# Performance work log

Hardware: AMD Instinct MI355X
Metric: run time of the kernel (lower is better)

## Reference

```python
import jax, jax.numpy as jnp
import numpy as np

# static sinkhorn parameters (match SamplesLoss init kwargs)
P = 2
BLUR = 0.05
SCALING = 0.5
DIAMETER = 2.0  # points on the unit sphere => diameter <= 2

# geomloss epsilon_schedule: [diameter^p] + exp(arange(p*log(d), p*log(blur), p*log(scaling))) + [blur^p]
EPS_LIST = (
    [DIAMETER ** P]
    + [float(np.exp(e)) for e in np.arange(P * np.log(DIAMETER), P * np.log(BLUR), P * np.log(SCALING))]
    + [BLUR ** P]
)


def cost(m, n):
    # spherical (geodesic) distance / 2 between unit vectors: acos(<m,n>)/2
    t = jnp.clip(jnp.einsum('bnd,bmd->bnm', m, n), -1.0 + 1e-6, 1.0 - 1e-6)
    return jnp.arccos(t) * 0.5  # (B,N,M)


def softmin(eps, C, wlog):
    # -eps * logsumexp(wlog[B,1,M] - C/eps, axis=2) -> (B,N)
    return -eps * jax.nn.logsumexp(wlog[:, None, :] - C / eps, axis=2)


def log_weights(a):
    return jnp.where(a > 0, jnp.log(jnp.maximum(a, 1e-30)), -1e5)


def setup_inputs() -> dict:
    key = jax.random.key(0)
    kx, ky = jax.random.split(key)
    B, N, M, D = 8, 2048, 2048, 3
    x = jax.random.normal(kx, (B, N, D), dtype=jnp.float32)
    y = jax.random.normal(ky, (B, M, D), dtype=jnp.float32)
    # project onto the unit sphere (spherical cost assumes unit vectors)
    x = x / jnp.linalg.norm(x, axis=-1, keepdims=True)
    y = y / jnp.linalg.norm(y, axis=-1, keepdims=True)
    alpha = jnp.ones((B, N), dtype=jnp.float32) / N
    beta = jnp.ones((B, M), dtype=jnp.float32) / M
    return {"alpha": alpha, "x": x, "beta": beta, "y": y}


def reference(alpha, x, beta, y):
    sg = jax.lax.stop_gradient
    # second argument of each cost is detached, as in the torch code
    C_xx = cost(x, sg(x))
    C_yy = cost(y, sg(y))
    C_xy = cost(x, sg(y))
    C_yx = cost(y, sg(x))
    al = log_weights(alpha)
    bl = log_weights(beta)

    # ---- sinkhorn loop (torch.no_grad section) ----
    Cxx_, Cyy_, Cxy_, Cyx_, al_, bl_ = map(sg, (C_xx, C_yy, C_xy, C_yx, al, bl))
    eps = EPS_LIST[0]
    a_x = softmin(eps, Cxx_, al_)   # OT(a,a) potential on x
    b_y = softmin(eps, Cyy_, bl_)   # OT(b,b) potential on y
    a_y = softmin(eps, Cyx_, al_)   # OT(a,b) potential on y
    b_x = softmin(eps, Cxy_, bl_)   # OT(a,b) potential on x
    for eps in EPS_LIST:  # annealed, symmetrized sinkhorn updates
        at_x = softmin(eps, Cxx_, al_ + a_x / eps)
        bt_y = softmin(eps, Cyy_, bl_ + b_y / eps)
        at_y = softmin(eps, Cyx_, al_ + b_x / eps)
        bt_x = softmin(eps, Cxy_, bl_ + a_y / eps)
        a_x, b_y = 0.5 * (a_x + at_x), 0.5 * (b_y + bt_y)
        a_y, b_x = 0.5 * (a_y + at_y), 0.5 * (b_x + bt_x)

    # ---- last extrapolation, differentiable (eps = blur^p) ----
    eps = EPS_LIST[-1]
    a_x = softmin(eps, C_xx, sg(al + a_x / eps))
    b_y = softmin(eps, C_yy, sg(bl + b_y / eps))
    a_y = softmin(eps, C_yx, sg(al + b_x / eps))
    b_x = softmin(eps, C_xy, sg(bl + a_y / eps))

    # balanced (reach=None), debiased sinkhorn cost -> (B,)
    return jnp.sum(alpha * (b_x - a_x), axis=-1) + jnp.sum(beta * (a_y - b_y), axis=-1)
```

## Files before the change

### kernel.cpp

```cpp
#include <hip/hip_runtime.h>
#include <math.h>

#define BB 8
#define NN 2048
#define L2E 1.4426950408889634f
#define LN2 0.6931471805599453f
#define PI_F 3.14159265358979f
#define CLIP 0.999999f
#define THSC 20860.0f
#define THSCI (1.0f / 20860.0f)

constexpr int TB   = 128;
constexpr int T16  = NN / TB;
constexpr int NXX  = T16 * (T16 + 1) / 2;
constexpr int NT   = 2 * NXX + T16 * T16;
constexpr int SARR = BB * NN;

__device__ __forceinline__ void decode_tile(int bx, int& kind, int& I, int& J) {
    if (bx < NXX) kind = 0;
    else if (bx < 2 * NXX) { kind = 1; bx -= NXX; }
    else { kind = 2; bx -= 2 * NXX; }
    if (kind < 2) {
        int idx = bx; I = 0;
        for (;;) { int len = T16 - I; if (idx < len) { J = I + idx; break; } idx -= len; I++; }
    } else { I = bx >> 4; J = bx & 15; }
}

__device__ __forceinline__ float acos_raw(float d) {
    const float u = fabsf(d);
    float pl = fmaf(u, -0.0187293f, 0.0742610f);
    pl = fmaf(u, pl, -0.2121144f); pl = fmaf(u, pl, 1.5707288f);
    const float rt = __builtin_amdgcn_sqrtf(1.f - u) * pl;
    return (d >= 0.f) ? rt : (PI_F - rt);
}

__device__ __forceinline__ size_t th_off(int g, int wv, int lane) {
    return (size_t)(((g * 4 + wv) * 64 + lane) * 8);
}

__global__ __launch_bounds__(256)
void pack_kernel(const float* __restrict__ alpha, const float* __restrict__ beta,
                 float* __restrict__ gxw, float* __restrict__ gyw,
                 float* __restrict__ Wall, float* __restrict__ Gall)
{
    const int tid = threadIdx.x;
    const int gid = blockIdx.x * 256 + tid;
    const int o = gid >> 14, i = gid & (SARR - 1);
    const float* w = (o == 0 || o == 3) ? alpha : beta;
    const float v = w[i];
    const float g = ((v > 0.f) ? logf(fmaxf(v, 1e-30f)) : -1e5f) * L2E;
    if (o == 0) gxw[i] = g;
    if (o == 1) gyw[i] = g;
    __shared__ float red[256];
    red[tid] = g;
    __syncthreads();
    const int base = tid & 128, loc = tid & 127;
    for (int st = 64; st; st >>= 1) {
        if (loc < st) red[base + loc] = fmaxf(red[base + loc], red[base + loc + st]);
        __syncthreads();
    }
    const float G = red[base];
    Wall[gid] = __builtin_amdgcn_exp2f(g - G);
    if (loc == 0) Gall[gid >> 7] = G;
}

__global__ __launch_bounds__(256)
void maxes_kernel(const float* __restrict__ x, const float* __restrict__ y,
                  float* __restrict__ Rxx, float* __restrict__ Ryy,
                  float* __restrict__ Rxy, float* __restrict__ Cxy,
                  unsigned short* __restrict__ Theta,
                  const float* __restrict__ Wall, const float* __restrict__ Gall,
                  float2* pAX, float2* pBY, float2* pAY, float2* pBX,
                  float negK, int writeTheta)
{
    __shared__ float4 p1s[TB], p2s[TB];
    __shared__ float colred[4][TB];
    __shared__ float colpart[4][TB];
    int kind, I, J; decode_tile(blockIdx.x, kind, I, J);
    const int b = blockIdx.y, t = threadIdx.x;
    const float* P1 = (kind == 1) ? y : x;
    const float* P2 = (kind == 0) ? x : y;
    const int o1 = (kind == 0) ? 0 : (kind == 1) ? 1 : 3;
    const int o2 = (kind == 0) ? 0 : (kind == 1) ? 1 : 2;
    float2* rowOut = (kind == 0) ? pAX : (kind == 1) ? pBY : pBX;
    float2* colOut = (kind == 0) ? pAX : (kind == 1) ? pBY : pAY;
    const bool diag = (kind < 2) && (I == J);
    const float* W1 = Wall + (size_t)o1 * SARR;
    const float* W2 = Wall + (size_t)o2 * SARR;

    if (t < TB) {
        size_t gi = (size_t)b * NN + (size_t)I * TB + t;
        p1s[t] = make_float4(P1[gi * 3], P1[gi * 3 + 1], P1[gi * 3 + 2], W1[gi]);
    } else {
        int u = t - TB; size_t gi = (size_t)b * NN + (size_t)J * TB + u;
        p2s[u] = make_float4(P2[gi * 3], P2[gi * 3 + 1], P2[gi * 3 + 2], W2[gi]);
    }
    const float G1 = Gall[o1 * 128 + b * T16 + I];
    const float G2 = Gall[o2 * 128 + b * T16 + J];
    __syncthreads();
    const int lane = t & 63, wv = t >> 6, colg = lane & 7, rowg = lane >> 3;
    const int r0 = wv * 32 + rowg * 4;
    unsigned short* Tb = Theta + ((size_t)(b * NT + blockIdx.x) << 14);

    float4 pr[4];
#pragma unroll
    for (int rr = 0; rr < 4; rr++) pr[rr] = p1s[r0 + rr];
    float rmx[4] = {-2.f, -2.f, -2.f, -2.f};
    float cmx[16];
#pragma unroll
    for (int j = 0; j < 16; j++) cmx[j] = -2.f;
    float racc[4] = {0.f, 0.f, 0.f, 0.f};
    float cacc[16];
#pragma unroll
    for (int j = 0; j < 16; j++) cacc[j] = 0.f;

#pragma unroll
    for (int g = 0; g < 8; g++) {
        uint4 outv;
#pragma unroll
        for (int e = 0; e < 2; e++) {
            const int j = g * 2 + e;
            const float4 q = p2s[colg + 8 * j];
            unsigned int lo = 0, hi = 0;
#pragma unroll
            for (int rr = 0; rr < 4; rr++) {
                const float d = fmaf(pr[rr].x, q.x, fmaf(pr[rr].y, q.y, pr[rr].z * q.z));
                rmx[rr] = fmaxf(rmx[rr], d);
                cmx[j] = fmaxf(cmx[j], d);
                if (writeTheta) {
                    const float dc = fminf(fmaxf(d, -CLIP), CLIP);
                    const float th = acos_raw(dc);
                    const unsigned int qv = __float2uint_rn(th * THSC);
                    if (rr == 0) lo = qv;
                    else if (rr == 1) lo |= qv << 16;
                    else if (rr == 2) hi = qv;
                    else hi |= qv << 16;
                    const float em = __builtin_amdgcn_exp2f(th * negK);
                    racc[rr] = fmaf(q.w, em, racc[rr]);
                    cacc[j]  = fmaf(pr[rr].w, em, cacc[j]);
                }
            }
            if (e == 0) { outv.x = lo; outv.y = hi; }
            else        { outv.z = lo; outv.w = hi; }
        }
        if (writeTheta)
            *(uint4*)(Tb + th_off(g, wv, lane)) = outv;
    }

#pragma unroll
    for (int rr = 0; rr < 4; rr++) {
        float v = rmx[rr];
        v = fmaxf(v, __shfl_xor(v, 1)); v = fmaxf(v, __shfl_xor(v, 2));
        v = fmaxf(v, __shfl_xor(v, 4));
        rmx[rr] = v;
    }
    if (colg == 0) {
        float* R = (kind == 0) ? Rxx : (kind == 1) ? Ryy : Rxy;
        const size_t base = ((size_t)b * T16 + J) * NN + (size_t)I * TB + r0;
#pragma unroll
        for (int rr = 0; rr < 4; rr++)
            R[base + rr] = acos_raw(fminf(fmaxf(rmx[rr], -CLIP), CLIP));
    }
#pragma unroll
    for (int j = 0; j < 16; j++) {
        float v = cmx[j];
        v = fmaxf(v, __shfl_xor(v, 8)); v = fmaxf(v, __shfl_xor(v, 16));
        v = fmaxf(v, __shfl_xor(v, 32));
        cmx[j] = v;
    }
    if (rowg == 0) {
#pragma unroll
        for (int j = 0; j < 16; j++) colred[wv][colg + 8 * j] = cmx[j];
    }

    if (writeTheta) {
#pragma unroll
        for (int j = 0; j < 16; j++) {
            float v = cacc[j];
            v += __shfl_xor(v, 8); v += __shfl_xor(v, 16); v += __shfl_xor(v, 32);
            cacc[j] = v;
        }
        if (rowg == 0) {
#pragma unroll
            for (int j = 0; j < 16; j++) colpart[wv][colg + 8 * j] = cacc[j];
        }
#pragma unroll
        for (int rr = 0; rr < 4; rr++) {
            float v = racc[rr];
            v += __shfl_xor(v, 1); v += __shfl_xor(v, 2); v += __shfl_xor(v, 4);
            racc[rr] = v;
        }
        if (colg == 0) {
            const size_t gr = (size_t)J * SARR + (size_t)b * NN + (size_t)I * TB + r0;
#pragma unroll
            for (int rr = 0; rr < 4; rr++)
                rowOut[gr + rr] = make_float2(G2, racc[rr]);
        }
    }

    __syncthreads();
    if (t < TB) {
        const float v = fmaxf(fmaxf(colred[0][t], colred[1][t]),
                              fmaxf(colred[2][t], colred[3][t]));
        const float th = acos_raw(fminf(fmaxf(v, -CLIP), CLIP));
        if (kind == 2) {
            Cxy[((size_t)b * T16 + I) * NN + (size_t)J * TB + t] = th;
        } else if (I != J) {
            float* R = (kind == 0) ? Rxx : Ryy;
            R[((size_t)b * T16 + I) * NN + (size_t)J * TB + t] = th;
        }
        if (writeTheta && !diag) {
            const float pv = colpart[0][t] + colpart[1][t] + colpart[2][t] + colpart[3][t];
            const size_t gc = (size_t)I * SARR + (size_t)b * NN + (size_t)J * TB + t;
            colOut[gc] = make_float2(G1, pv);
        }
    }
}

struct TileArgsT {
    const unsigned short* Theta;
    const float* Wall; const float* Gall;
    const float* Rxx; const float* Ryy; const float* Rxy; const float* Cxy;
    float2* pAX; float2* pBY; float2* pAY; float2* pBX;
};

__global__ __launch_bounds__(256)
void tile_theta_kernel(TileArgsT A, float ieh, float Kq)
{
    __shared__ float2 s1[TB];
    __shared__ float2 wq2[TB];
    __shared__ float  scF[TB];
    __shared__ float  wps[TB];
    __shared__ float colpart[4][TB];
    int kind, I, J; decode_tile(blockIdx.x, kind, I, J);
    const int b = blockIdx.y, t = threadIdx.x;
    const int o1 = (kind == 0) ? 0 : (kind == 1) ? 1 : 3;
    const int o2 = (kind == 0) ? 0 : (kind == 1) ? 1 : 2;
    float2* rowOut = (kind == 0) ? A.pAX : (kind == 1) ? A.pBY : A.pBX;
    float2* colOut = (kind == 0) ? A.pAX : (kind == 1) ? A.pBY : A.pAY;
    const bool diag = (kind < 2) && (I == J);
    const float* W1 = A.Wall + (size_t)o1 * SARR;
    const float* W2 = A.Wall + (size_t)o2 * SARR;
    const float* Rrow = (kind == 0) ? A.Rxx : (kind == 1) ? A.Ryy : A.Rxy;
    const float* Csrc = (kind == 0) ? A.Rxx : (kind == 1) ? A.Ryy : A.Cxy;

    float myW = 0.f, mySc = 0.f;
    if (t < TB) {
        size_t gi = (size_t)b * NN + (size_t)I * TB + t;
        myW = W1[gi];
        s1[t] = make_float2(Rrow[((size_t)b * T16 + J) * NN + (size_t)I * TB + t] * ieh, myW);
    } else {
        int u = t - TB; size_t gi = (size_t)b * NN + (size_t)J * TB + u;
        myW = W2[gi];
        mySc = Csrc[((size_t)b * T16 + I) * NN + (size_t)J * TB + u] * ieh;
        scF[u] = mySc;
    }
    const float G1 = A.Gall[o1 * 128 + b * T16 + I];
    const float G2 = A.Gall[o2 * 128 + b * T16 + J];
    __syncthreads();
    const float Z2 = 0.5f * s1[0].x;
    if (t < TB) {
        wps[t] = myW * __builtin_amdgcn_exp2f(Z2 - 0.5f * s1[t].x);
    } else {
        int u = t - TB;
        wq2[u] = make_float2(0.5f * mySc,
                             myW * __builtin_amdgcn_exp2f(Z2 - 0.5f * mySc));
    }
    __syncthreads();

    const int lane = t & 63, wv = t >> 6, colg = lane & 7, rowg = lane >> 3;
    const int r0 = wv * 32 + rowg * 4;
    const unsigned short* Tb = A.Theta + ((size_t)(b * NT + blockIdx.x) << 14);

    float srrF[4], srr2[4], wpr[4];
#pragma unroll
    for (int rr = 0; rr < 4; rr++) {
        srrF[rr] = s1[r0 + rr].x;
        srr2[rr] = 0.5f * srrF[rr];
        wpr[rr]  = wps[r0 + rr];
    }
    float racc[4] = {0.f, 0.f, 0.f, 0.f};
    float cacc[16];
#pragma unroll
    for (int j = 0; j < 16; j++) cacc[j] = 0.f;

#pragma unroll
    for (int g = 0; g < 8; g++) {
        const uint4 tq = *(const uint4*)(Tb + th_off(g, wv, lane));
#pragma unroll
        for (int e = 0; e < 2; e++) {
            const int j = g * 2 + e;
            const unsigned int lo = e ? tq.z : tq.x;
            const unsigned int hi = e ? tq.w : tq.y;
            const float2 q2 = wq2[colg + 8 * j];
            const float thv[4] = {
                (float)(lo & 0xffffu), (float)(lo >> 16),
                (float)(hi & 0xffffu), (float)(hi >> 16)
            };
            float bs[4];
#pragma unroll
            for (int rr = 0; rr < 4; rr++) bs[rr] = srr2[rr] + q2.x;
#pragma unroll
            for (int rr = 0; rr < 4; rr++) {
                const float em = __builtin_amdgcn_exp2f(fmaf(thv[rr], -Kq, bs[rr]));
                racc[rr] = fmaf(q2.y, em, racc[rr]);
                cacc[j]  = fmaf(wpr[rr], em, cacc[j]);
            }
        }
    }

#pragma unroll
    for (int j = 0; j < 16; j++) {
        float v = cacc[j];
        v += __shfl_xor(v, 8); v += __shfl_xor(v, 16); v += __shfl_xor(v, 32);
        cacc[j] = v;
    }
    if (rowg == 0) {
#pragma unroll
        for (int j = 0; j < 16; j++) {
            const int c = colg + 8 * j;
            colpart[wv][c] = cacc[j] * __builtin_amdgcn_exp2f(wq2[c].x - Z2);
        }
    }
#pragma unroll
    for (int rr = 0; rr < 4; rr++) {
        float v = racc[rr];
        v += __shfl_xor(v, 1); v += __shfl_xor(v, 2); v += __shfl_xor(v, 4);
        racc[rr] = v;
    }
    if (colg == 0) {
        const size_t gr = (size_t)J * SARR + (size_t)b * NN + (size_t)I * TB + r0;
#pragma unroll
        for (int rr = 0; rr < 4; rr++)
            rowOut[gr + rr] = make_float2(G2 - srrF[rr],
                racc[rr] * __builtin_amdgcn_exp2f(srr2[rr] - Z2));
    }
    __syncthreads();
    if (!diag && t < TB) {
        const float v = colpart[0][t] + colpart[1][t] + colpart[2][t] + colpart[3][t];
        const size_t gc = (size_t)I * SARR + (size_t)b * NN + (size_t)J * TB + t;
        colOut[gc] = make_float2(G1 - scF[t], v);
    }
}

struct TileArgs {
    const float* x; const float* y;
    const float* Wall; const float* Gall;
    const float* Rxx; const float* Ryy; const float* Rxy; const float* Cxy;
    float2* pAX; float2* pBY; float2* pAY; float2* pBX;
};

__global__ __launch_bounds__(256)
void tile_kernel(TileArgs A, float ieh, float pi_ieh)
{
    __shared__ float4 p1s[TB], p2s[TB];
    __shared__ float srs[TB], scs[TB];
    __shared__ float colpart[4][TB];
    int kind, I, J; decode_tile(blockIdx.x, kind, I, J);
    const int b = blockIdx.y, t = threadIdx.x;
    const float* P1 = (kind == 1) ? A.y : A.x;
    const float* P2 = (kind == 0) ? A.x : A.y;
    const int o1 = (kind == 0) ? 0 : (kind == 1) ? 1 : 3;
    const int o2 = (kind == 0) ? 0 : (kind == 1) ? 1 : 2;
    float2* rowOut = (kind == 0) ? A.pAX : (kind == 1) ? A.pBY : A.pBX;
    float2* colOut = (kind == 0) ? A.pAX : (kind == 1) ? A.pBY : A.pAY;
    const bool diag = (kind < 2) && (I == J);
    const float* W1 = A.Wall + (size_t)o1 * SARR;
    const float* W2 = A.Wall + (size_t)o2 * SARR;
    const float* Rrow = (kind == 0) ? A.Rxx : (kind == 1) ? A.Ryy : A.Rxy;
    const float* Csrc = (kind == 0) ? A.Rxx : (kind == 1) ? A.Ryy : A.Cxy;

    const float K0 = 1.5707288f * ieh, K1 = -0.2121144f * ieh;
    const float K2 = 0.0742610f * ieh, K3 = -0.0187293f * ieh;

    if (t < TB) {
        size_t gi = (size_t)b * NN + (size_t)I * TB + t;
        p1s[t] = make_float4(P1[gi * 3], P1[gi * 3 + 1], P1[gi * 3 + 2], W1[gi]);
        srs[t] = Rrow[((size_t)b * T16 + J) * NN + (size_t)I * TB + t] * ieh;
    } else {
        int u = t - TB; size_t gi = (size_t)b * NN + (size_t)J * TB + u;
        p2s[u] = make_float4(P2[gi * 3], P2[gi * 3 + 1], P2[gi * 3 + 2], W2[gi]);
        scs[u] = Csrc[((size_t)b * T16 + I) * NN + (size_t)J * TB + u] * ieh;
    }
    const float G1 = A.Gall[o1 * 128 + b * T16 + I];
    const float G2 = A.Gall[o2 * 128 + b * T16 + J];
    __syncthreads();

    const int lane = t & 63, wv = t >> 6, colg = lane & 7, rowg = lane >> 3;
    const int r0 = wv * 32 + rowg * 4;
    float4 pr[4]; float srr[4];
#pragma unroll
    for (int rr = 0; rr < 4; rr++) { pr[rr] = p1s[r0 + rr]; srr[rr] = srs[r0 + rr]; }
    float racc[4] = {0.f, 0.f, 0.f, 0.f};
    float cacc[16];
#pragma unroll
    for (int j = 0; j < 16; j++) cacc[j] = 0.f;

#pragma unroll
    for (int j = 0; j < 16; j++) {
        const float4 q = p2s[colg + 8 * j];
        const float sc = scs[colg + 8 * j];
#pragma unroll
        for (int rr = 0; rr < 4; rr++) {
            const float4 p = pr[rr];
            float d = fmaf(p.x, q.x, fmaf(p.y, q.y, p.z * q.z));
            d = fminf(fmaxf(d, -CLIP), CLIP);
            const float u = fabsf(d);
            float pl = fmaf(u, K3, K2); pl = fmaf(u, pl, K1); pl = fmaf(u, pl, K0);
            const float rt = __builtin_amdgcn_sqrtf(1.f - u) * pl;
            const float ach = (d >= 0.f) ? rt : (pi_ieh - rt);
            racc[rr] = fmaf(q.w, __builtin_amdgcn_exp2f(srr[rr] - ach), racc[rr]);
            cacc[j]  = fmaf(p.w, __builtin_amdgcn_exp2f(sc - ach), cacc[j]);
        }
    }

#pragma unroll
    for (int j = 0; j < 16; j++) {
        float v = cacc[j];
        v += __shfl_xor(v, 8); v += __shfl_xor(v, 16); v += __shfl_xor(v, 32);
        cacc[j] = v;
    }
    if (rowg == 0) {
#pragma unroll
        for (int j = 0; j < 16; j++) colpart[wv][colg + 8 * j] = cacc[j];
    }
#pragma unroll
    for (int rr = 0; rr < 4; rr++) {
        float v = racc[rr];
        v += __shfl_xor(v, 1); v += __shfl_xor(v, 2); v += __shfl_xor(v, 4);
        racc[rr] = v;
    }
    if (colg == 0) {
        const size_t gr = (size_t)J * SARR + (size_t)b * NN + (size_t)I * TB + r0;
#pragma unroll
        for (int rr = 0; rr < 4; rr++)
            rowOut[gr + rr] = make_float2(G2 - srr[rr], racc[rr]);
    }
    __syncthreads();
    if (!diag && t < TB) {
        const float v = colpart[0][t] + colpart[1][t] + colpart[2][t] + colpart[3][t];
        const size_t gc = (size_t)I * SARR + (size_t)b * NN + (size_t)J * TB + t;
        colOut[gc] = make_float2(G1 - scs[t], v);
    }
}

__global__ __launch_bounds__(256)
void combine_kernel(const float2* __restrict__ pAX, const float2* __restrict__ pBY,
                    const float2* __restrict__ pAY, const float2* __restrict__ pBX,
                    float* __restrict__ ax, float* __restrict__ by,
                    float* __restrict__ ay, float* __restrict__ bx,
                    const float* __restrict__ gxw, const float* __restrict__ gyw,
                    float* __restrict__ Wall, float* __restrict__ Gall,
                    float eps_ln2, float nieL2E, int do_avg)
{
    const int tid = threadIdx.x;
    const int gid = blockIdx.x * 256 + tid;
    const int o = gid >> 14, i = gid & (SARR - 1);
    const float2* P = (o == 0) ? pAX : (o == 1) ? pBY : (o == 2) ? pAY : pBX;
    float* pot = (o == 0) ? ax : (o == 1) ? by : (o == 2) ? ay : bx;
    float2 pr[T16];
#pragma unroll
    for (int u = 0; u < T16; u++) pr[u] = P[(size_t)u * SARR + i];
    float M = -3.0e38f;
#pragma unroll
    for (int u = 0; u < T16; u++) M = fmaxf(M, (pr[u].y > 0.f) ? pr[u].x : -3.0e38f);
    float S = 0.f;
#pragma unroll
    for (int u = 0; u < T16; u++)
        S += pr[u].y * __builtin_amdgcn_exp2f(fminf(pr[u].x - M, 0.f));
    S = fmaxf(S, 1e-38f);
    float r = -eps_ln2 * (M + __builtin_amdgcn_logf(S));
    if (do_avg) r = 0.5f * (r + pot[i]);
    pot[i] = r;
    const float g = ((o == 0 || o == 3) ? gxw[i] : gyw[i]) + r * nieL2E;
    __shared__ float red[256];
    red[tid] = g;
    __syncthreads();
    const int base = tid & 128, loc = tid & 127;
    for (int st = 64; st; st >>= 1) {
        if (loc < st) red[base + loc] = fmaxf(red[base + loc], red[base + loc + st]);
        __syncthreads();
    }
    const float G = red[base];
    Wall[gid] = __builtin_amdgcn_exp2f(g - G);
    if (loc == 0) Gall[gid >> 7] = G;
}

__global__ __launch_bounds__(256)
void reduce_kernel(const float* __restrict__ alpha, const float* __restrict__ beta,
                   const float* __restrict__ a_x, const float* __restrict__ b_x,
                   const float* __restrict__ a_y, const float* __restrict__ b_y,
                   float* __restrict__ out)
{
    const int b = blockIdx.x, tid = threadIdx.x;
    float acc = 0.f;
    for (int n = tid; n < NN; n += 256) {
        const size_t i = (size_t)b * NN + n;
        acc += alpha[i] * (b_x[i] - a_x[i]);
        acc += beta[i] * (a_y[i] - b_y[i]);
    }
    __shared__ float red[256];
    red[tid] = acc;
    __syncthreads();
    for (int st = 128; st > 0; st >>= 1) {
        if (tid < st) red[tid] += red[tid + st];
        __syncthreads();
    }
    if (tid == 0) out[b] = red[0];
}

extern "C" void kernel_launch(void* const* d_in, const int* in_sizes, int n_in,
                              void* d_out, int out_size, void* d_ws, size_t ws_size,
                              hipStream_t stream)
{
    const float* alpha = (const float*)d_in[0];
    const float* x     = (const float*)d_in[1];
    const float* beta  = (const float*)d_in[2];
    const float* y     = (const float*)d_in[3];
    float* out = (float*)d_out;
    float* ws  = (float*)d_ws;

    const size_t S = SARR;
    float* gxw  = ws;
    float* gyw  = ws + S;
    float* ax   = ws + 2 * S;
    float* by   = ws + 3 * S;
    float* ay   = ws + 4 * S;
    float* bx   = ws + 5 * S;
    float* Wall = ws + 6 * S;
    float* Gall = ws + 10 * S;
    float* Rxx  = ws + 10 * S + 512;
    float* Ryy  = Rxx + 16 * S;
    float* Rxy  = Ryy + 16 * S;
    float* Cxy  = Rxy + 16 * S;
    float* pb   = Cxy + 16 * S;
    const size_t PSZ = (size_t)SARR * T16;
    float2* pAX = (float2*)pb;
    float2* pBY = pAX + PSZ;
    float2* pAY = pBY + PSZ;
    float2* pBX = pAY + PSZ;

    float* thetaF = pb + (size_t)8 * PSZ;
    unsigned short* Theta = (unsigned short*)thetaF;
    const size_t used_bytes  = (size_t)((char*)thetaF - (char*)ws);
    const size_t theta_bytes = (size_t)BB * NT * 16384 * sizeof(unsigned short);
    const int useTheta = (ws_size >= used_bytes + theta_bytes) ? 1 : 0;

    const float EPS[8] = {4.0f, 4.0f, 1.0f, 0.25f, 0.0625f, 0.015625f, 0.00390625f, 0.0025f};

    pack_kernel<<<(4 * SARR) / 256, 256, 0, stream>>>(alpha, beta, gxw, gyw, Wall, Gall);
    const float negK = -0.5f * (1.f / EPS[0]) * L2E;
    maxes_kernel<<<dim3(NT, BB), 256, 0, stream>>>(x, y, Rxx, Ryy, Rxy, Cxy, Theta,
                                                   Wall, Gall, pAX, pBY, pAY, pBX,
                                                   negK, useTheta);

    TileArgsT TT;
    TT.Theta = Theta; TT.Wall = Wall; TT.Gall = Gall;
    TT.Rxx = Rxx; TT.Ryy = Ryy; TT.Rxy = Rxy; TT.Cxy = Cxy;
    TT.pAX = pAX; TT.pBY = pBY; TT.pAY = pAY; TT.pBX = pBX;

    TileArgs TA;
    TA.x = x; TA.y = y; TA.Wall = Wall; TA.Gall = Gall;
    TA.Rxx = Rxx; TA.Ryy = Ryy; TA.Rxy = Rxy; TA.Cxy = Cxy;
    TA.pAX = pAX; TA.pBY = pBY; TA.pAY = pAY; TA.pBX = pBX;

    auto step = [&](float e, float next_e, int avg, int run_tile) {
        const float ieh = 0.5f * (1.f / e) * L2E;
        if (run_tile) {
            if (useTheta)
                tile_theta_kernel<<<dim3(NT, BB), 256, 0, stream>>>(TT, ieh, ieh * THSCI);
            else
                tile_kernel<<<dim3(NT, BB), 256, 0, stream>>>(TA, ieh, PI_F * ieh);
        }
        combine_kernel<<<(4 * SARR) / 256, 256, 0, stream>>>(
            pAX, pBY, pAY, pBX, ax, by, ay, bx, gxw, gyw, Wall, Gall,
            e * LN2, (1.f / next_e) * L2E, avg);
    };

    step(EPS[0], EPS[0], 0, useTheta ? 0 : 1);
    for (int k = 0; k < 8; k++) step(EPS[k], (k < 7) ? EPS[k + 1] : EPS[7], 1, 1);
    step(EPS[7], EPS[7], 0, 1);

    reduce_kernel<<<BB, 256, 0, stream>>>(alpha, beta, ax, bx, ay, by, out);
}
```

Baseline: 451.8 us.

## Use wave-shuffle max reductions and drop the rank-one exponent factorization in theta tiles

```diff
diff --git a/kernel.cpp b/kernel.cpp
--- a/kernel.cpp
+++ b/kernel.cpp
@@ -51,17 +51,18 @@
     const float g = ((v > 0.f) ? logf(fmaxf(v, 1e-30f)) : -1e5f) * L2E;
     if (o == 0) gxw[i] = g;
     if (o == 1) gyw[i] = g;
-    __shared__ float red[256];
-    red[tid] = g;
-    __syncthreads();
-    const int base = tid & 128, loc = tid & 127;
-    for (int st = 64; st; st >>= 1) {
-        if (loc < st) red[base + loc] = fmaxf(red[base + loc], red[base + loc + st]);
-        __syncthreads();
-    }
-    const float G = red[base];
+    float m = g;
+    m = fmaxf(m, __shfl_xor(m, 1));  m = fmaxf(m, __shfl_xor(m, 2));
+    m = fmaxf(m, __shfl_xor(m, 4));  m = fmaxf(m, __shfl_xor(m, 8));
+    m = fmaxf(m, __shfl_xor(m, 16)); m = fmaxf(m, __shfl_xor(m, 32));
+    __shared__ float wmax[4];
+    const int wv = tid >> 6;
+    if ((tid & 63) == 0) wmax[wv] = m;
+    __syncthreads();
+    const int grp = tid >> 7;
+    const float G = fmaxf(wmax[grp * 2], wmax[grp * 2 + 1]);
     Wall[gid] = __builtin_amdgcn_exp2f(g - G);
-    if (loc == 0) Gall[gid >> 7] = G;
+    if ((tid & 127) == 0) Gall[gid >> 7] = G;
 }
 
 __global__ __launch_bounds__(256)
@@ -227,10 +228,7 @@
 __global__ __launch_bounds__(256)
 void tile_theta_kernel(TileArgsT A, float ieh, float Kq)
 {
-    __shared__ float2 s1[TB];
-    __shared__ float2 wq2[TB];
-    __shared__ float  scF[TB];
-    __shared__ float  wps[TB];
+    __shared__ float2 s1[TB], s2[TB];
     __shared__ float colpart[4][TB];
     int kind, I, J; decode_tile(blockIdx.x, kind, I, J);
     const int b = blockIdx.y, t = threadIdx.x;
@@ -244,41 +242,24 @@
     const float* Rrow = (kind == 0) ? A.Rxx : (kind == 1) ? A.Ryy : A.Rxy;
     const float* Csrc = (kind == 0) ? A.Rxx : (kind == 1) ? A.Ryy : A.Cxy;
 
-    float myW = 0.f, mySc = 0.f;
     if (t < TB) {
         size_t gi = (size_t)b * NN + (size_t)I * TB + t;
-        myW = W1[gi];
-        s1[t] = make_float2(Rrow[((size_t)b * T16 + J) * NN + (size_t)I * TB + t] * ieh, myW);
+        s1[t] = make_float2(Rrow[((size_t)b * T16 + J) * NN + (size_t)I * TB + t] * ieh, W1[gi]);
     } else {
         int u = t - TB; size_t gi = (size_t)b * NN + (size_t)J * TB + u;
-        myW = W2[gi];
-        mySc = Csrc[((size_t)b * T16 + I) * NN + (size_t)J * TB + u] * ieh;
-        scF[u] = mySc;
+        s2[u] = make_float2(Csrc[((size_t)b * T16 + I) * NN + (size_t)J * TB + u] * ieh, W2[gi]);
     }
     const float G1 = A.Gall[o1 * 128 + b * T16 + I];
     const float G2 = A.Gall[o2 * 128 + b * T16 + J];
-    __syncthreads();
-    const float Z2 = 0.5f * s1[0].x;
-    if (t < TB) {
-        wps[t] = myW * __builtin_amdgcn_exp2f(Z2 - 0.5f * s1[t].x);
-    } else {
-        int u = t - TB;
-        wq2[u] = make_float2(0.5f * mySc,
-                             myW * __builtin_amdgcn_exp2f(Z2 - 0.5f * mySc));
-    }
     __syncthreads();
 
     const int lane = t & 63, wv = t >> 6, colg = lane & 7, rowg = lane >> 3;
     const int r0 = wv * 32 + rowg * 4;
     const unsigned short* Tb = A.Theta + ((size_t)(b * NT + blockIdx.x) << 14);
 
-    float srrF[4], srr2[4], wpr[4];
-#pragma unroll
-    for (int rr = 0; rr < 4; rr++) {
-        srrF[rr] = s1[r0 + rr].x;
-        srr2[rr] = 0.5f * srrF[rr];
-        wpr[rr]  = wps[r0 + rr];
-    }
+    float srr[4], w1r[4];
+#pragma unroll
+    for (int rr = 0; rr < 4; rr++) { const float2 v = s1[r0 + rr]; srr[rr] = v.x; w1r[rr] = v.y; }
     float racc[4] = {0.f, 0.f, 0.f, 0.f};
     float cacc[16];
 #pragma unroll
@@ -292,19 +273,17 @@
             const int j = g * 2 + e;
             const unsigned int lo = e ? tq.z : tq.x;
             const unsigned int hi = e ? tq.w : tq.y;
-            const float2 q2 = wq2[colg + 8 * j];
+            const float2 sv = s2[colg + 8 * j];
             const float thv[4] = {
                 (float)(lo & 0xffffu), (float)(lo >> 16),
                 (float)(hi & 0xffffu), (float)(hi >> 16)
             };
-            float bs[4];
-#pragma unroll
-            for (int rr = 0; rr < 4; rr++) bs[rr] = srr2[rr] + q2.x;
 #pragma unroll
             for (int rr = 0; rr < 4; rr++) {
-                const float em = __builtin_amdgcn_exp2f(fmaf(thv[rr], -Kq, bs[rr]));
-                racc[rr] = fmaf(q2.y, em, racc[rr]);
-                cacc[j]  = fmaf(wpr[rr], em, cacc[j]);
+                const float er = __builtin_amdgcn_exp2f(fmaf(thv[rr], -Kq, srr[rr]));
+                const float ec = __builtin_amdgcn_exp2f(fmaf(thv[rr], -Kq, sv.x));
+                racc[rr] = fmaf(sv.y, er, racc[rr]);
+                cacc[j]  = fmaf(w1r[rr], ec, cacc[j]);
             }
         }
     }
@@ -317,10 +296,7 @@
     }
     if (rowg == 0) {
 #pragma unroll
-        for (int j = 0; j < 16; j++) {
-            const int c = colg + 8 * j;
-            colpart[wv][c] = cacc[j] * __builtin_amdgcn_exp2f(wq2[c].x - Z2);
-        }
+        for (int j = 0; j < 16; j++) colpart[wv][colg + 8 * j] = cacc[j];
     }
 #pragma unroll
     for (int rr = 0; rr < 4; rr++) {
@@ -332,14 +308,13 @@
         const size_t gr = (size_t)J * SARR + (size_t)b * NN + (size_t)I * TB + r0;
 #pragma unroll
         for (int rr = 0; rr < 4; rr++)
-            rowOut[gr + rr] = make_float2(G2 - srrF[rr],
-                racc[rr] * __builtin_amdgcn_exp2f(srr2[rr] - Z2));
+            rowOut[gr + rr] = make_float2(G2 - srr[rr], racc[rr]);
     }
     __syncthreads();
     if (!diag && t < TB) {
         const float v = colpart[0][t] + colpart[1][t] + colpart[2][t] + colpart[3][t];
         const size_t gc = (size_t)I * SARR + (size_t)b * NN + (size_t)J * TB + t;
-        colOut[gc] = make_float2(G1 - scF[t], v);
+        colOut[gc] = make_float2(G1 - s2[t].x, v);
     }
 }
 
@@ -473,17 +448,18 @@
     if (do_avg) r = 0.5f * (r + pot[i]);
     pot[i] = r;
     const float g = ((o == 0 || o == 3) ? gxw[i] : gyw[i]) + r * nieL2E;
-    __shared__ float red[256];
-    red[tid] = g;
-    __syncthreads();
-    const int base = tid & 128, loc = tid & 127;
-    for (int st = 64; st; st >>= 1) {
-        if (loc < st) red[base + loc] = fmaxf(red[base + loc], red[base + loc + st]);
-        __syncthreads();
-    }
-    const float G = red[base];
+    float m = g;
+    m = fmaxf(m, __shfl_xor(m, 1));  m = fmaxf(m, __shfl_xor(m, 2));
+    m = fmaxf(m, __shfl_xor(m, 4));  m = fmaxf(m, __shfl_xor(m, 8));
+    m = fmaxf(m, __shfl_xor(m, 16)); m = fmaxf(m, __shfl_xor(m, 32));
+    __shared__ float wmax[4];
+    const int wv = tid >> 6;
+    if ((tid & 63) == 0) wmax[wv] = m;
+    __syncthreads();
+    const int grp = tid >> 7;
+    const float G = fmaxf(wmax[grp * 2], wmax[grp * 2 + 1]);
     Wall[gid] = __builtin_amdgcn_exp2f(g - G);
-    if (loc == 0) Gall[gid >> 7] = G;
+    if ((tid & 127) == 0) Gall[gid >> 7] = G;
 }
 
 __global__ __launch_bounds__(256)
```

Measured after the change: 412.4 us. -8.7%, faster.
